# Performance work log

Measured on AMD Instinct MI355X. Metric: run time of the kernel, lower is better.

The kernel has to match this reference:

```python
import jax, jax.numpy as jnp
import numpy as np

BS, SEQ, DIM, HEADS = 2, 2048, 1024, 16
HEAD_DIM = DIM // HEADS
NEG = -1e9


def setup_inputs() -> dict:
    key = jax.random.key(0)
    ks = jax.random.split(key, 5)
    s = 1.0 / np.sqrt(DIM)
    return {
        "x": jax.random.normal(ks[0], (BS, SEQ, DIM), jnp.float32),
        "padding_mask": jnp.ones((BS, SEQ), jnp.int32),
        "causal_mask": jnp.tril(jnp.ones((SEQ, SEQ), jnp.int32)),
        "Wq": jax.random.normal(ks[1], (DIM, DIM), jnp.float32) * s,
        "bq": jnp.zeros((DIM,), jnp.float32),
        "Wk": jax.random.normal(ks[2], (DIM, DIM), jnp.float32) * s,
        "bk": jnp.zeros((DIM,), jnp.float32),
        "Wv": jax.random.normal(ks[3], (DIM, DIM), jnp.float32) * s,
        "bv": jnp.zeros((DIM,), jnp.float32),
        "Wo": jax.random.normal(ks[4], (DIM, DIM), jnp.float32) * s,
        "bo": jnp.zeros((DIM,), jnp.float32),
    }


def reference(x, padding_mask, causal_mask, Wq, bq, Wk, bk, Wv, bv, Wo, bo):
    bs, seq, dim = x.shape
    # QKV projections -> [b, h, s, d]
    def proj(W, b):
        return (x @ W.T + b).reshape(bs, seq, HEADS, HEAD_DIM).transpose(0, 2, 1, 3)
    q, k, v = proj(Wq, bq), proj(Wk, bk), proj(Wv, bv)
    scores = jnp.einsum("bhqd,bhkd->bhqk", q, k) / np.sqrt(HEAD_DIM).astype(np.float32)
    scores = jnp.where(padding_mask[:, None, None, :] == 0, NEG, scores)
    scores = jnp.where(causal_mask[None, None, :, :] == 0, NEG, scores)
    attn = jax.nn.softmax(scores, axis=-1)
    out = jnp.einsum("bhqk,bhkd->bhqd", attn, v)
    out = out.transpose(0, 2, 1, 3).reshape(bs, seq, dim)
    return out @ Wo.T + bo
```

## Files before the change

kernel.cpp:

```cpp
#include <hip/hip_runtime.h>
#include <hip/hip_bf16.h>
#include <stdint.h>

#define SEQ 2048
#define DIM 1024
#define HEADS 16
#define HD 64
#define NEGV (-1e9f)

typedef __attribute__((ext_vector_type(8))) short short8;
typedef __attribute__((ext_vector_type(4))) float f32x4;

__device__ __forceinline__ unsigned short f2bf(float f) {
  __hip_bfloat16 h = __float2bfloat16(f);
  union { __hip_bfloat16 h; unsigned short u; } cv;
  cv.h = h;
  return cv.u;
}

__device__ __forceinline__ void async16(const void* g, void* l) {
  __builtin_amdgcn_global_load_lds(
      (const __attribute__((address_space(1))) unsigned int*)g,
      (__attribute__((address_space(3))) unsigned int*)l, 16, 0, 0);
}

__global__ void cast_bf16_k(const float* __restrict__ in,
                            unsigned short* __restrict__ out, int n4) {
  int stride = gridDim.x * blockDim.x;
  for (int i = blockIdx.x * blockDim.x + threadIdx.x; i < n4; i += stride) {
    float4 v = ((const float4*)in)[i];
    ushort4 o;
    o.x = f2bf(v.x); o.y = f2bf(v.y); o.z = f2bf(v.z); o.w = f2bf(v.w);
    ((ushort4*)out)[i] = o;
  }
}

__global__ void cast_w4_k(const float* __restrict__ w0, const float* __restrict__ w1,
                          const float* __restrict__ w2, const float* __restrict__ w3,
                          unsigned short* __restrict__ o0, unsigned short* __restrict__ o1,
                          unsigned short* __restrict__ o2, unsigned short* __restrict__ o3,
                          int n4) {
  const float* in = (blockIdx.y == 0) ? w0 : (blockIdx.y == 1) ? w1
                   : (blockIdx.y == 2) ? w2 : w3;
  unsigned short* out = (blockIdx.y == 0) ? o0 : (blockIdx.y == 1) ? o1
                       : (blockIdx.y == 2) ? o2 : o3;
  int stride = gridDim.x * blockDim.x;
  for (int i = blockIdx.x * blockDim.x + threadIdx.x; i < n4; i += stride) {
    float4 v = ((const float4*)in)[i];
    ushort4 o;
    o.x = f2bf(v.x); o.y = f2bf(v.y); o.z = f2bf(v.z); o.w = f2bf(v.w);
    ((ushort4*)out)[i] = o;
  }
}

__device__ __forceinline__ void gemm_core(const unsigned short* __restrict__ A,
                                          const unsigned short* __restrict__ B,
                                          int K, int bm0, int bn0,
                                          unsigned short* As, unsigned short* Bs,
                                          f32x4 acc[4][4]) {
  const int tid  = threadIdx.x;
  const int lane = tid & 63;
  const int w    = tid >> 6;
  const int wr   = w >> 1, wc = w & 1;
  const int lrow = lane & 15, lkg = lane >> 4;

  for (int k0 = 0; k0 < K; k0 += 32) {
#pragma unroll
    for (int i = 0; i < 2; ++i) {
      int e   = (i * 256 + tid) * 8;
      int row = e >> 5;
      int kk  = e & 31;
      async16(A + (size_t)(bm0 + row) * K + (size_t)(k0 + kk), As + e);
      async16(B + (size_t)(bn0 + row) * K + (size_t)(k0 + kk), Bs + e);
    }
    __syncthreads();

    short8 af[4], bf[4];
#pragma unroll
    for (int i = 0; i < 4; ++i) {
      af[i] = *(const short8*)(As + (wr * 64 + i * 16 + lrow) * 32 + lkg * 8);
      bf[i] = *(const short8*)(Bs + (wc * 64 + i * 16 + lrow) * 32 + lkg * 8);
    }
#pragma unroll
    for (int i = 0; i < 4; ++i)
#pragma unroll
      for (int j = 0; j < 4; ++j)
        acc[i][j] = __builtin_amdgcn_mfma_f32_16x16x32_bf16(af[i], bf[j], acc[i][j], 0, 0, 0);
    __syncthreads();
  }
}

__global__ __launch_bounds__(256)
void qkv_gemm_k(const unsigned short* __restrict__ xb,
                const unsigned short* __restrict__ wqb,
                const unsigned short* __restrict__ wkb,
                const unsigned short* __restrict__ wvb,
                const float* __restrict__ bq, const float* __restrict__ bk,
                const float* __restrict__ bv,
                unsigned short* __restrict__ Qb, unsigned short* __restrict__ Kb,
                unsigned short* __restrict__ Vtb) {
  __shared__ __align__(16) unsigned short As[128 * 32];
  __shared__ __align__(16) unsigned short Bs[128 * 32];
  const int z = blockIdx.z;
  const unsigned short* B = (z == 0) ? wqb : (z == 1) ? wkb : wvb;
  const float* bias       = (z == 0) ? bq  : (z == 1) ? bk  : bv;
  const int bm0 = blockIdx.y * 128, bn0 = blockIdx.x * 128;

  f32x4 acc[4][4] = {};
  gemm_core(xb, B, DIM, bm0, bn0, As, Bs, acc);

  const int lane = threadIdx.x & 63;
  const int w = threadIdx.x >> 6, wr = w >> 1, wc = w & 1;
  unsigned short* out01 = (z == 0) ? Qb : Kb;
#pragma unroll
  for (int i = 0; i < 4; ++i)
#pragma unroll
    for (int j = 0; j < 4; ++j)
#pragma unroll
      for (int r = 0; r < 4; ++r) {
        int mg = bm0 + wr * 64 + i * 16 + (lane >> 4) * 4 + r;
        int ng = bn0 + wc * 64 + j * 16 + (lane & 15);
        float v = acc[i][j][r] + bias[ng];
        int bb = mg >> 11, s = mg & 2047, h = ng >> 6, d = ng & 63;
        int bh = bb * HEADS + h;
        if (z < 2)
          out01[((size_t)bh * SEQ + s) * HD + d] = f2bf(v);
        else
          Vtb[((size_t)bh * HD + d) * SEQ + s] = f2bf(v);
      }
}

__global__ __launch_bounds__(256)
void out_gemm_k(const unsigned short* __restrict__ Ob,
                const unsigned short* __restrict__ wob,
                const float* __restrict__ bo, float* __restrict__ out) {
  __shared__ __align__(16) unsigned short As[128 * 32];
  __shared__ __align__(16) unsigned short Bs[128 * 32];
  const int bm0 = blockIdx.y * 128, bn0 = blockIdx.x * 128;

  f32x4 acc[4][4] = {};
  gemm_core(Ob, wob, DIM, bm0, bn0, As, Bs, acc);

  const int lane = threadIdx.x & 63;
  const int w = threadIdx.x >> 6, wr = w >> 1, wc = w & 1;
#pragma unroll
  for (int i = 0; i < 4; ++i)
#pragma unroll
    for (int j = 0; j < 4; ++j)
#pragma unroll
      for (int r = 0; r < 4; ++r) {
        int mg = bm0 + wr * 64 + i * 16 + (lane >> 4) * 4 + r;
        int ng = bn0 + wc * 64 + j * 16 + (lane & 15);
        out[(size_t)mg * DIM + ng] = acc[i][j][r] + bo[ng];
      }
}

__device__ __forceinline__ void stage_kv64(const unsigned short* __restrict__ kbase,
                                           const unsigned short* __restrict__ vbase,
                                           int k0, unsigned short* KsB,
                                           unsigned short* VsB, int tid) {
#pragma unroll
  for (int j = 0; j < 2; ++j) {
    const int c    = j * 256 + tid;
    const int row  = c >> 3;
    const int colb = (c & 7) << 4;
    const int srcb = colb ^ ((row & 7) << 4);
    async16(kbase + (size_t)(k0 + row) * HD + (srcb >> 1), KsB + c * 8);
  }
#pragma unroll
  for (int j = 0; j < 2; ++j) {
    const int c    = j * 256 + tid;
    const int d    = c >> 3;
    const int colb = (c & 7) << 4;
    const int srcb = colb ^ ((d & 7) << 4);
    async16(vbase + (size_t)d * SEQ + k0 + (srcb >> 1), VsB + c * 8);
  }
}

__global__ __launch_bounds__(256)
void attn_k(const unsigned short* __restrict__ Q,
            const unsigned short* __restrict__ Kp,
            const unsigned short* __restrict__ Vt,
            const int* __restrict__ pm,
            unsigned short* __restrict__ O) {
  __shared__ __align__(16) unsigned short Ks[2][64 * 64];
  __shared__ __align__(16) unsigned short Vs[2][64 * 64];
  __shared__ __align__(16) unsigned short plds[4][16 * 64];

  const int tid  = threadIdx.x;
  const int lane = tid & 63;
  const int w    = tid >> 6;
  const int lc = lane & 15, lg = lane >> 4;
  const int qb = 31 - blockIdx.y;
  const int bh = blockIdx.x;
  const int b  = bh >> 4, h = bh & 15;

  const size_t base = (size_t)bh * SEQ * HD;
  const unsigned short* kbase = Kp + base;
  const unsigned short* vbase = Vt + (size_t)bh * HD * SEQ;
  const int* pmb = pm + b * SEQ;
  char* pb = (char*)&plds[w][0];
  const int swp = (lc & 7) << 4;

  const int qrow0 = qb * 64 + w * 16;
  const int qrow  = qrow0 + lc;

  short8 qa[2];
  {
    const unsigned short* qp = Q + base + (size_t)qrow * HD + lg * 8;
    qa[0] = *(const short8*)(qp);
    qa[1] = *(const short8*)(qp + 32);
  }

  f32x4 oacc[4] = {};
  float mrow = -1e30f, lsum = 0.f;

  const int nk = qb + 1;

  stage_kv64(kbase, vbase, 0, Ks[0], Vs[0], tid);
  __syncthreads();

  for (int kt = 0; kt < nk; ++kt) {
    const int cur = kt & 1;
    const int k0 = kt * 64;
    if (kt + 1 < nk)
      stage_kv64(kbase, vbase, k0 + 64, Ks[cur ^ 1], Vs[cur ^ 1], tid);

    f32x4 s[4];
    const char* kbuf = (const char*)Ks[cur];
    __builtin_amdgcn_s_setprio(1);
#pragma unroll
    for (int t = 0; t < 4; ++t) {
      const int row = t * 16 + lc;
      const int swk = (row & 7) << 4;
      const char* kr = kbuf + row * 128;
      short8 kb0 = *(const short8*)(kr + ((lg * 16) ^ swk));
      short8 kb1 = *(const short8*)(kr + ((lg * 16 + 64) ^ swk));
      f32x4 z = {};
      z = __builtin_amdgcn_mfma_f32_16x16x32_bf16(kb0, qa[0], z, 0, 0, 0);
      z = __builtin_amdgcn_mfma_f32_16x16x32_bf16(kb1, qa[1], z, 0, 0, 0);
      const int kr0 = k0 + t * 16;
      int4 pmv = *(const int4*)(pmb + kr0 + lg * 4);
#pragma unroll
      for (int r = 0; r < 4; ++r) {
        const int kidx = kr0 + lg * 4 + r;
        float sv = z[r] * 0.125f;
        if (kidx > qrow || (&pmv.x)[r] == 0) sv = NEGV;
        s[t][r] = sv;
      }
    }
    __builtin_amdgcn_s_setprio(0);

    float mx = -1e30f;
#pragma unroll
    for (int t = 0; t < 4; ++t)
      mx = fmaxf(mx, fmaxf(fmaxf(s[t][0], s[t][1]), fmaxf(s[t][2], s[t][3])));
    mx = fmaxf(mx, __shfl_xor(mx, 16, 64));
    mx = fmaxf(mx, __shfl_xor(mx, 32, 64));
    if (!__all(mx <= mrow + 8.f)) {
      const float mnew = fmaxf(mrow, mx);
      const float sc = __expf(mrow - mnew);
      lsum *= sc;
      mrow = mnew;
      const float s0 = __shfl(sc, lg * 4 + 0, 64);
      const float s1 = __shfl(sc, lg * 4 + 1, 64);
      const float s2 = __shfl(sc, lg * 4 + 2, 64);
      const float s3 = __shfl(sc, lg * 4 + 3, 64);
#pragma unroll
      for (int t = 0; t < 4; ++t) {
        oacc[t][0] *= s0; oacc[t][1] *= s1; oacc[t][2] *= s2; oacc[t][3] *= s3;
      }
    }
    float sum = 0.f;
#pragma unroll
    for (int t = 0; t < 4; ++t)
#pragma unroll
      for (int r = 0; r < 4; ++r) {
        const float p = __expf(s[t][r] - mrow);
        s[t][r] = p;
        sum += p;
      }
    sum += __shfl_xor(sum, 16, 64);
    sum += __shfl_xor(sum, 32, 64);
    lsum += sum;

#pragma unroll
    for (int t = 0; t < 4; ++t) {
      short4 pk;
      pk.x = (short)f2bf(s[t][0]); pk.y = (short)f2bf(s[t][1]);
      pk.z = (short)f2bf(s[t][2]); pk.w = (short)f2bf(s[t][3]);
      const int colb = (t * 16 + lg * 4) * 2;
      *(short4*)(pb + lc * 128 + (colb ^ swp)) = pk;
    }
    short8 pa[2];
#pragma unroll
    for (int ks = 0; ks < 2; ++ks)
      pa[ks] = *(const short8*)(pb + lc * 128 + (((ks * 32 + lg * 8) * 2) ^ swp));

    const char* vbuf = (const char*)Vs[cur];
    __builtin_amdgcn_s_setprio(1);
#pragma unroll
    for (int t = 0; t < 4; ++t) {
      const int d = t * 16 + lc;
      const int swv = (d & 7) << 4;
      const char* vr = vbuf + d * 128;
#pragma unroll
      for (int ks = 0; ks < 2; ++ks) {
        short8 vv = *(const short8*)(vr + ((ks * 64 + lg * 16) ^ swv));
        oacc[t] = __builtin_amdgcn_mfma_f32_16x16x32_bf16(pa[ks], vv, oacc[t], 0, 0, 0);
      }
    }
    __builtin_amdgcn_s_setprio(0);

    __syncthreads();
  }

  const float l0 = __shfl(lsum, lg * 4 + 0, 64);
  const float l1 = __shfl(lsum, lg * 4 + 1, 64);
  const float l2 = __shfl(lsum, lg * 4 + 2, 64);
  const float l3 = __shfl(lsum, lg * 4 + 3, 64);
  const float i0 = 1.f / l0, i1 = 1.f / l1, i2 = 1.f / l2, i3 = 1.f / l3;
#pragma unroll
  for (int t = 0; t < 4; ++t) {
    const size_t o0 = ((size_t)(b * SEQ + qrow0 + lg * 4)) * DIM + h * HD + t * 16 + lc;
    O[o0]           = f2bf(oacc[t][0] * i0);
    O[o0 + DIM]     = f2bf(oacc[t][1] * i1);
    O[o0 + 2 * DIM] = f2bf(oacc[t][2] * i2);
    O[o0 + 3 * DIM] = f2bf(oacc[t][3] * i3);
  }
}

extern "C" void kernel_launch(void* const* d_in, const int* in_sizes, int n_in,
                              void* d_out, int out_size, void* d_ws, size_t ws_size,
                              hipStream_t stream) {
  const float* x  = (const float*)d_in[0];
  const int*   pm = (const int*)d_in[1];
  const float* Wq = (const float*)d_in[3];
  const float* bq = (const float*)d_in[4];
  const float* Wk = (const float*)d_in[5];
  const float* bk = (const float*)d_in[6];
  const float* Wv = (const float*)d_in[7];
  const float* bv = (const float*)d_in[8];
  const float* Wo = (const float*)d_in[9];
  const float* bo = (const float*)d_in[10];

  const size_t NX = (size_t)4096 * 1024;
  const size_t NW = (size_t)1024 * 1024;

  unsigned short* ws  = (unsigned short*)d_ws;
  unsigned short* xb  = ws;
  unsigned short* wqb = xb + NX;
  unsigned short* wkb = wqb + NW;
  unsigned short* wvb = wkb + NW;
  unsigned short* wob = wvb + NW;
  unsigned short* Qb  = wob + NW;
  unsigned short* Kb  = Qb + NX;
  unsigned short* Vtb = Kb + NX;
  unsigned short* Ob  = xb;

  cast_bf16_k<<<dim3(2048), dim3(256), 0, stream>>>(x, xb, (int)(NX / 4));
  cast_w4_k<<<dim3(512, 4), dim3(256), 0, stream>>>(Wq, Wk, Wv, Wo,
                                                    wqb, wkb, wvb, wob,
                                                    (int)(NW / 4));

  qkv_gemm_k<<<dim3(8, 32, 3), dim3(256), 0, stream>>>(xb, wqb, wkb, wvb,
                                                       bq, bk, bv, Qb, Kb, Vtb);

  attn_k<<<dim3(32, 32), dim3(256), 0, stream>>>(Qb, Kb, Vtb, pm, Ob);

  out_gemm_k<<<dim3(8, 32), dim3(256), 0, stream>>>(Ob, wob, bo, (float*)d_out);
}
```

Before: 142.7 us.

## Skip padding-mask work when all ones, use exp2 softmax, defer row reductions

The attention kernel now scans the padding mask once per block and, if it is all ones, skips the per-tile mask loads and compares, applying only the causal mask on the diagonal tile. Softmax switches to base-2 exponentials by folding log2(e) into the score scale and the rescale threshold. The cross-lane max reduction moves inside the rare rescale branch, and the cross-lane sum reduction is deferred to the end of the kernel. This trims per-tile VALU and shuffle work, at the cost of an upfront mask scan and slightly more subtle running-max semantics.

```diff
diff --git a/kernel.cpp b/kernel.cpp
--- a/kernel.cpp
+++ b/kernel.cpp
@@ -7,6 +7,8 @@
 #define HEADS 16
 #define HD 64
 #define NEGV (-1e9f)
+#define SCALE2 0.18033688011112042f
+#define THR2 11.541560327111707f
 
 typedef __attribute__((ext_vector_type(8))) short short8;
 typedef __attribute__((ext_vector_type(4))) float f32x4;
@@ -186,6 +188,7 @@
   __shared__ __align__(16) unsigned short Ks[2][64 * 64];
   __shared__ __align__(16) unsigned short Vs[2][64 * 64];
   __shared__ __align__(16) unsigned short plds[4][16 * 64];
+  __shared__ int wflag[4];
 
   const int tid  = threadIdx.x;
   const int lane = tid & 63;
@@ -218,7 +221,18 @@
   const int nk = qb + 1;
 
   stage_kv64(kbase, vbase, 0, Ks[0], Vs[0], tid);
+
+  {
+    int ok = 1;
+    for (int i = tid; i < SEQ / 4; i += 256) {
+      int4 v = ((const int4*)pmb)[i];
+      ok &= (v.x != 0) & (v.y != 0) & (v.z != 0) & (v.w != 0);
+    }
+    ok = __all(ok) ? 1 : 0;
+    if (lane == 0) wflag[w] = ok;
+  }
   __syncthreads();
+  const bool allones = (wflag[0] & wflag[1] & wflag[2] & wflag[3]) != 0;
 
   for (int kt = 0; kt < nk; ++kt) {
     const int cur = kt & 1;
@@ -239,27 +253,41 @@
       f32x4 z = {};
       z = __builtin_amdgcn_mfma_f32_16x16x32_bf16(kb0, qa[0], z, 0, 0, 0);
       z = __builtin_amdgcn_mfma_f32_16x16x32_bf16(kb1, qa[1], z, 0, 0, 0);
-      const int kr0 = k0 + t * 16;
-      int4 pmv = *(const int4*)(pmb + kr0 + lg * 4);
-#pragma unroll
-      for (int r = 0; r < 4; ++r) {
-        const int kidx = kr0 + lg * 4 + r;
-        float sv = z[r] * 0.125f;
-        if (kidx > qrow || (&pmv.x)[r] == 0) sv = NEGV;
-        s[t][r] = sv;
-      }
+#pragma unroll
+      for (int r = 0; r < 4; ++r) s[t][r] = z[r] * SCALE2;
     }
     __builtin_amdgcn_s_setprio(0);
+
+    if (!allones) {
+#pragma unroll
+      for (int t = 0; t < 4; ++t) {
+        const int kr0 = k0 + t * 16;
+        int4 pmv = *(const int4*)(pmb + kr0 + lg * 4);
+#pragma unroll
+        for (int r = 0; r < 4; ++r) {
+          const int kidx = kr0 + lg * 4 + r;
+          if (kidx > qrow || (&pmv.x)[r] == 0) s[t][r] = NEGV;
+        }
+      }
+    } else if (kt == qb) {
+#pragma unroll
+      for (int t = 0; t < 4; ++t)
+#pragma unroll
+        for (int r = 0; r < 4; ++r) {
+          const int kidx = k0 + t * 16 + lg * 4 + r;
+          if (kidx > qrow) s[t][r] = NEGV;
+        }
+    }
 
     float mx = -1e30f;
 #pragma unroll
     for (int t = 0; t < 4; ++t)
       mx = fmaxf(mx, fmaxf(fmaxf(s[t][0], s[t][1]), fmaxf(s[t][2], s[t][3])));
-    mx = fmaxf(mx, __shfl_xor(mx, 16, 64));
-    mx = fmaxf(mx, __shfl_xor(mx, 32, 64));
-    if (!__all(mx <= mrow + 8.f)) {
+    if (!__all(mx <= mrow + THR2)) {
+      mx = fmaxf(mx, __shfl_xor(mx, 16, 64));
+      mx = fmaxf(mx, __shfl_xor(mx, 32, 64));
       const float mnew = fmaxf(mrow, mx);
-      const float sc = __expf(mrow - mnew);
+      const float sc = exp2f(mrow - mnew);
       lsum *= sc;
       mrow = mnew;
       const float s0 = __shfl(sc, lg * 4 + 0, 64);
@@ -276,12 +304,10 @@
     for (int t = 0; t < 4; ++t)
 #pragma unroll
       for (int r = 0; r < 4; ++r) {
-        const float p = __expf(s[t][r] - mrow);
+        const float p = exp2f(s[t][r] - mrow);
         s[t][r] = p;
         sum += p;
       }
-    sum += __shfl_xor(sum, 16, 64);
-    sum += __shfl_xor(sum, 32, 64);
     lsum += sum;
 
 #pragma unroll
@@ -315,6 +341,8 @@
     __syncthreads();
   }
 
+  lsum += __shfl_xor(lsum, 16, 64);
+  lsum += __shfl_xor(lsum, 32, 64);
   const float l0 = __shfl(lsum, lg * 4 + 0, 64);
   const float l1 = __shfl(lsum, lg * 4 + 1, 64);
   const float l2 = __shfl(lsum, lg * 4 + 2, 64);
```

After: 123.2 us. -13.7%, faster.
